# Kernel tuning notes

Hardware: AMD Instinct MI355X
Metric: run time of the kernel (lower is better)

Reference implementation:

```python
import jax, jax.numpy as jnp
import numpy as np

BLOCK = 128


def setup_inputs() -> dict:
    key = jax.random.key(0)
    k_x, k_w, k_s, k_b = jax.random.split(key, 4)
    B, S, IN, OUT = 2, 2048, 4096, 4096
    x = jax.random.normal(k_x, (B, S, IN), dtype=jnp.float32)
    # fp8-quantized weight values (simulate e4m3 rounding, keep fp32 storage)
    w = jax.random.normal(k_w, (OUT, IN), dtype=jnp.float32) * 0.02
    weight = w.astype(jnp.float8_e4m3fn).astype(jnp.float32)
    # per-128x128-block inverse scales
    weight_scale_inv = jax.random.uniform(
        k_s, (OUT // BLOCK, IN // BLOCK), dtype=jnp.float32, minval=0.5, maxval=1.5)
    bias = jax.random.normal(k_b, (OUT,), dtype=jnp.float32) * 0.01
    return {"x": x, "weight": weight, "weight_scale_inv": weight_scale_inv, "bias": bias}


def _dequant(weight, scale_inv):
    # weight: [O, I], scale_inv: [O/128, I/128] -> broadcast each scale over a 128x128 block
    O, I = weight.shape
    w = weight.reshape(O // BLOCK, BLOCK, I // BLOCK, BLOCK)
    w = w * scale_inv[:, None, :, None]
    return w.reshape(O, I)


def reference(x, weight, weight_scale_inv, bias):
    w_deq = _dequant(weight, weight_scale_inv)          # [O, I]
    out = jnp.einsum('bsi,oi->bso', x, w_deq)           # [B, S, O]
    return out + bias
```

## Files before the change

kernel.cpp:

```cpp
#include <hip/hip_runtime.h>
#include <hip/hip_bf16.h>
#include <stdint.h>

typedef __attribute__((ext_vector_type(4))) float f32x4;
typedef __attribute__((ext_vector_type(8))) short short8;

__device__ __forceinline__ ushort f2b(float f) {
    union { __hip_bfloat16 h; ushort u; } c;
    c.h = __float2bfloat16(f);
    return c.u;
}

__device__ __forceinline__ void gload_lds16(const void* g, void* lds) {
    __builtin_amdgcn_global_load_lds((const __attribute__((address_space(1))) void*)g,
                                     (__attribute__((address_space(3))) void*)lds,
                                     16, 0, 0);
}

#define BARRIER()  asm volatile("s_barrier" ::: "memory")
#define LGKM0()    asm volatile("s_waitcnt lgkmcnt(0)" ::: "memory")
#define VMCNT2()   asm volatile("s_waitcnt vmcnt(2)" ::: "memory")

__global__ void conv_x_kernel(const float* __restrict__ x, ushort* __restrict__ xb, long n8) {
    long i = (long)blockIdx.x * blockDim.x + threadIdx.x;
    if (i >= n8) return;
    const float4* xv = (const float4*)x;
    float4 v0 = xv[i * 2], v1 = xv[i * 2 + 1];
    short8 r;
    r[0] = (short)f2b(v0.x); r[1] = (short)f2b(v0.y); r[2] = (short)f2b(v0.z); r[3] = (short)f2b(v0.w);
    r[4] = (short)f2b(v1.x); r[5] = (short)f2b(v1.y); r[6] = (short)f2b(v1.z); r[7] = (short)f2b(v1.w);
    *(short8*)&xb[i * 8] = r;
}

__global__ void conv_w_kernel(const float* __restrict__ w, const float* __restrict__ sinv,
                              ushort* __restrict__ wb, int K, int nbk) {
    const int o = blockIdx.y;
    const int c = (blockIdx.x * blockDim.x + threadIdx.x) * 8;
    if (c >= K) return;
    const float s = sinv[(o >> 7) * nbk + (c >> 7)];
    const float4* wv = (const float4*)(w + (size_t)o * K + c);
    float4 v0 = wv[0], v1 = wv[1];
    short8 r;
    r[0] = (short)f2b(v0.x * s); r[1] = (short)f2b(v0.y * s); r[2] = (short)f2b(v0.z * s); r[3] = (short)f2b(v0.w * s);
    r[4] = (short)f2b(v1.x * s); r[5] = (short)f2b(v1.y * s); r[6] = (short)f2b(v1.z * s); r[7] = (short)f2b(v1.w * s);
    *(short8*)&wb[(size_t)o * K + c] = r;
}

__global__ __launch_bounds__(512, 2)
void gemm256_kernel(const ushort* __restrict__ A, const ushort* __restrict__ Bm,
                    const float* __restrict__ bias, float* __restrict__ C,
                    int M, int N, int K) {
    __shared__ alignas(16) short sm[2][32768];

    const int tid  = threadIdx.x;
    const int lane = tid & 63;
    const int wid  = tid >> 6;
    const int wr   = wid >> 2;
    const int wc   = wid & 3;
    const int nbn  = N >> 8;

    const int nwg = gridDim.x;
    const int swz = (blockIdx.x & 7) * (nwg >> 3) + (blockIdx.x >> 3);
    const int bm  = swz / nbn;
    const int bn  = swz % nbn;

    const short* gA = (const short*)A + (size_t)bm * 256 * K;
    const short* gB = (const short*)Bm + (size_t)bn * 256 * K;

    const int srow = wid * 8 + (lane >> 3);
    const int scol = ((lane & 7) ^ (lane >> 3)) << 3;

    auto STAGE_A = [&](int U, int kt, int buf) {
        const short* src = gA + (size_t)(U * 64 + srow) * K + kt * 64 + scol;
        gload_lds16(src, &sm[buf][U * 4096 + wid * 512]);
    };
    auto STAGE_B = [&](int U, int kt, int buf) {
        const short* src = gB + (size_t)(U * 64 + srow) * K + kt * 64 + scol;
        gload_lds16(src, &sm[buf][16384 + U * 4096 + wid * 512]);
    };

    auto LD_A = [&](const short* Ab, int mh, int kk, short8 (&a)[4]) {
#pragma unroll
        for (int m = 0; m < 4; ++m) {
            int row = wr * 128 + mh * 64 + m * 16 + (lane & 15);
            a[m] = *(const short8*)&Ab[row * 64 + ((kk * 32 + (lane >> 4) * 8) ^ ((lane & 7) << 3))];
        }
    };
    auto LD_B = [&](const short* Bb, int kk, short8 (&b)[4]) {
#pragma unroll
        for (int n = 0; n < 4; ++n) {
            int row = wc * 64 + n * 16 + (lane & 15);
            b[n] = *(const short8*)&Bb[row * 64 + ((kk * 32 + (lane >> 4) * 8) ^ ((lane & 7) << 3))];
        }
    };

    f32x4 acc[8][4] = {};
    const int nkt = K >> 6;

    auto KSTEP = [&](int t) {
        const int b  = t & 1;
        const int tb = b ^ 1;
        const short* Ab = &sm[b][0];
        const short* Bb = &sm[b][16384];
        const int tn  = (t + 1 < nkt) ? t + 1 : nkt - 1;
        const int tnn = (t + 2 < nkt) ? t + 2 : nkt - 1;

        short8 a0[4], a1[4], bf0[4], bf1[4];

        LD_A(Ab, 0, 0, a0);
        LD_B(Bb, 0, bf0);
        STAGE_B(0, tn, tb); STAGE_B(1, tn, tb);
        BARRIER();
        LGKM0();
        __builtin_amdgcn_s_setprio(1);
#pragma unroll
        for (int m = 0; m < 4; ++m)
#pragma unroll
            for (int n = 0; n < 4; ++n)
                acc[m][n] = __builtin_amdgcn_mfma_f32_16x16x32_bf16(a0[m], bf0[n], acc[m][n], 0, 0, 0);
        __builtin_amdgcn_s_setprio(0);
        BARRIER();

        LD_A(Ab, 1, 0, a1);
        STAGE_A(2, tn, tb); STAGE_A(3, tn, tb);
        BARRIER();
        LGKM0();
        __builtin_amdgcn_s_setprio(1);
#pragma unroll
        for (int m = 0; m < 4; ++m)
#pragma unroll
            for (int n = 0; n < 4; ++n)
                acc[4 + m][n] = __builtin_amdgcn_mfma_f32_16x16x32_bf16(a1[m], bf0[n], acc[4 + m][n], 0, 0, 0);
        __builtin_amdgcn_s_setprio(0);
        BARRIER();

        LD_A(Ab, 0, 1, a0);
        LD_B(Bb, 1, bf1);
        STAGE_B(2, tn, tb); STAGE_B(3, tn, tb);
        BARRIER();
        LGKM0();
        __builtin_amdgcn_s_setprio(1);
#pragma unroll
        for (int m = 0; m < 4; ++m)
#pragma unroll
            for (int n = 0; n < 4; ++n)
                acc[m][n] = __builtin_amdgcn_mfma_f32_16x16x32_bf16(a0[m], bf1[n], acc[m][n], 0, 0, 0);
        __builtin_amdgcn_s_setprio(0);
        BARRIER();

        LD_A(Ab, 1, 1, a1);
        STAGE_A(0, tnn, b); STAGE_A(1, tnn, b);
        BARRIER();
        LGKM0();
        __builtin_amdgcn_s_setprio(1);
#pragma unroll
        for (int m = 0; m < 4; ++m)
#pragma unroll
            for (int n = 0; n < 4; ++n)
                acc[4 + m][n] = __builtin_amdgcn_mfma_f32_16x16x32_bf16(a1[m], bf1[n], acc[4 + m][n], 0, 0, 0);
        __builtin_amdgcn_s_setprio(0);
        VMCNT2();
        BARRIER();
    };

    {
        STAGE_B(0, 0, 0); STAGE_B(1, 0, 0);
        STAGE_A(2, 0, 0); STAGE_A(3, 0, 0);
        STAGE_B(2, 0, 0); STAGE_B(3, 0, 0);
        STAGE_A(0, 0, 0); STAGE_A(1, 0, 0);
        const int t1 = (nkt > 1) ? 1 : 0;
        STAGE_A(0, t1, 1); STAGE_A(1, t1, 1);
        VMCNT2();
        BARRIER();
    }

    for (int t = 0; t < nkt; t += 2) {
        KSTEP(t);
        KSTEP(t + 1);
    }

    const int r0 = bm * 256 + wr * 128 + (lane >> 4) * 4;
    const int c0 = bn * 256 + wc * 64 + (lane & 15);
#pragma unroll
    for (int n = 0; n < 4; ++n) {
        float bv = bias[c0 + n * 16];
#pragma unroll
        for (int m = 0; m < 8; ++m) {
#pragma unroll
            for (int r = 0; r < 4; ++r) {
                C[(size_t)(r0 + m * 16 + r) * N + (c0 + n * 16)] = acc[m][n][r] + bv;
            }
        }
    }
}

__global__ void fallback_gemm(const float* __restrict__ x, const float* __restrict__ w,
                              const float* __restrict__ sinv, const float* __restrict__ bias,
                              float* __restrict__ out, int M, int N, int K) {
    int n = blockIdx.x * 64 + (threadIdx.x & 63);
    int m = blockIdx.y * 4 + (threadIdx.x >> 6);
    if (m >= M || n >= N) return;
    const int nbk = K >> 7;
    float acc = 0.f;
    for (int k = 0; k < K; ++k)
        acc += x[(size_t)m * K + k] * w[(size_t)n * K + k] * sinv[(n >> 7) * nbk + (k >> 7)];
    out[(size_t)m * N + n] = acc + bias[n];
}

extern "C" void kernel_launch(void* const* d_in, const int* in_sizes, int n_in,
                              void* d_out, int out_size, void* d_ws, size_t ws_size,
                              hipStream_t stream) {
    const float* x    = (const float*)d_in[0];
    const float* w    = (const float*)d_in[1];
    const float* sinv = (const float*)d_in[2];
    const float* bias = (const float*)d_in[3];
    float* out        = (float*)d_out;

    const int O = in_sizes[3];
    const int K = in_sizes[1] / O;
    const int M = (int)((long)in_sizes[0] / K);
    const int N = O;

    const size_t need = ((size_t)M * K + (size_t)N * K) * sizeof(ushort);
    const int nwg = (M / 256) * (N / 256);
    const bool ok = ws_size >= need && (M % 256 == 0) && (N % 256 == 0) &&
                    (K % 128 == 0) && (nwg % 8 == 0) && ((long)M * K % 2048 == 0) &&
                    (K % 2048 == 0);
    if (ok) {
        ushort* xb = (ushort*)d_ws;
        ushort* wb = xb + (size_t)M * K;
        long n8 = (long)M * K / 8;
        conv_x_kernel<<<dim3((unsigned)(n8 / 256)), 256, 0, stream>>>(x, xb, n8);
        conv_w_kernel<<<dim3(K / 2048, N), 256, 0, stream>>>(w, sinv, wb, K, K >> 7);
        gemm256_kernel<<<dim3(nwg), 512, 0, stream>>>(xb, wb, bias, out, M, N, K);
    } else {
        dim3 g(N / 64, (M + 3) / 4);
        fallback_gemm<<<g, 256, 0, stream>>>(x, w, sinv, bias, out, M, N, K);
    }
}
```

Baseline: 281.4 us.

## Interleave LDS fragment loads with MFMAs and halve barriers per k-step

Rebuilds the GEMM main-loop schedule. Each k-step now uses four barriers instead of eight, and the explicit lgkmcnt(0) waits are gone. LDS fragment reads for the next sub-tile are issued between halves of the current MFMA block, so LDS latency hides behind matrix math. A-tile staging is regrouped so units 0/2 and 1/3 are refilled at the points where they are no longer read. This cuts sync stalls but depends on the compiler's waitcnt insertion and on subtle buffer-reuse ordering staying correct.

```diff
diff --git a/kernel.cpp b/kernel.cpp
--- a/kernel.cpp
+++ b/kernel.cpp
@@ -18,7 +18,6 @@
 }
 
 #define BARRIER()  asm volatile("s_barrier" ::: "memory")
-#define LGKM0()    asm volatile("s_waitcnt lgkmcnt(0)" ::: "memory")
 #define VMCNT2()   asm volatile("s_waitcnt vmcnt(2)" ::: "memory")
 
 __global__ void conv_x_kernel(const float* __restrict__ x, ushort* __restrict__ xb, long n8) {
@@ -95,6 +94,15 @@
     };
 
     f32x4 acc[8][4] = {};
+
+    auto MFMA_H = [&](int off, short8 (&af)[4], short8 (&bf)[4], int m0, int m1) {
+#pragma unroll
+        for (int m = m0; m < m1; ++m)
+#pragma unroll
+            for (int n = 0; n < 4; ++n)
+                acc[off + m][n] = __builtin_amdgcn_mfma_f32_16x16x32_bf16(af[m], bf[n], acc[off + m][n], 0, 0, 0);
+    };
+
     const int nkt = K >> 6;
 
     auto KSTEP = [&](int t) {
@@ -105,73 +113,51 @@
         const int tn  = (t + 1 < nkt) ? t + 1 : nkt - 1;
         const int tnn = (t + 2 < nkt) ? t + 2 : nkt - 1;
 
-        short8 a0[4], a1[4], bf0[4], bf1[4];
-
-        LD_A(Ab, 0, 0, a0);
-        LD_B(Bb, 0, bf0);
+        short8 aA[4], aB[4], aC[4], aD[4], bA[4], bB[4];
+
+        BARRIER();
+        LD_A(Ab, 0, 0, aA);
+        LD_B(Bb, 0, bA);
+        __builtin_amdgcn_s_setprio(1);
+        MFMA_H(0, aA, bA, 0, 2);
+        LD_A(Ab, 1, 0, aB);
+        MFMA_H(0, aA, bA, 2, 4);
+        __builtin_amdgcn_s_setprio(0);
         STAGE_B(0, tn, tb); STAGE_B(1, tn, tb);
-        BARRIER();
-        LGKM0();
-        __builtin_amdgcn_s_setprio(1);
-#pragma unroll
-        for (int m = 0; m < 4; ++m)
-#pragma unroll
-            for (int n = 0; n < 4; ++n)
-                acc[m][n] = __builtin_amdgcn_mfma_f32_16x16x32_bf16(a0[m], bf0[n], acc[m][n], 0, 0, 0);
-        __builtin_amdgcn_s_setprio(0);
-        BARRIER();
-
-        LD_A(Ab, 1, 0, a1);
-        STAGE_A(2, tn, tb); STAGE_A(3, tn, tb);
-        BARRIER();
-        LGKM0();
-        __builtin_amdgcn_s_setprio(1);
-#pragma unroll
-        for (int m = 0; m < 4; ++m)
-#pragma unroll
-            for (int n = 0; n < 4; ++n)
-                acc[4 + m][n] = __builtin_amdgcn_mfma_f32_16x16x32_bf16(a1[m], bf0[n], acc[4 + m][n], 0, 0, 0);
-        __builtin_amdgcn_s_setprio(0);
-        BARRIER();
-
-        LD_A(Ab, 0, 1, a0);
-        LD_B(Bb, 1, bf1);
+
+        BARRIER();
+        __builtin_amdgcn_s_setprio(1);
+        MFMA_H(4, aB, bA, 0, 2);
+        LD_A(Ab, 0, 1, aC);
+        LD_B(Bb, 1, bB);
+        MFMA_H(4, aB, bA, 2, 4);
+        __builtin_amdgcn_s_setprio(0);
+        STAGE_A(1, tn, tb); STAGE_A(3, tn, tb);
+
+        BARRIER();
+        __builtin_amdgcn_s_setprio(1);
+        MFMA_H(0, aC, bB, 0, 2);
+        LD_A(Ab, 1, 1, aD);
+        MFMA_H(0, aC, bB, 2, 4);
+        __builtin_amdgcn_s_setprio(0);
         STAGE_B(2, tn, tb); STAGE_B(3, tn, tb);
-        BARRIER();
-        LGKM0();
-        __builtin_amdgcn_s_setprio(1);
-#pragma unroll
-        for (int m = 0; m < 4; ++m)
-#pragma unroll
-            for (int n = 0; n < 4; ++n)
-                acc[m][n] = __builtin_amdgcn_mfma_f32_16x16x32_bf16(a0[m], bf1[n], acc[m][n], 0, 0, 0);
-        __builtin_amdgcn_s_setprio(0);
-        BARRIER();
-
-        LD_A(Ab, 1, 1, a1);
-        STAGE_A(0, tnn, b); STAGE_A(1, tnn, b);
-        BARRIER();
-        LGKM0();
-        __builtin_amdgcn_s_setprio(1);
-#pragma unroll
-        for (int m = 0; m < 4; ++m)
-#pragma unroll
-            for (int n = 0; n < 4; ++n)
-                acc[4 + m][n] = __builtin_amdgcn_mfma_f32_16x16x32_bf16(a1[m], bf1[n], acc[4 + m][n], 0, 0, 0);
-        __builtin_amdgcn_s_setprio(0);
+
+        BARRIER();
+        __builtin_amdgcn_s_setprio(1);
+        MFMA_H(4, aD, bB, 0, 4);
+        __builtin_amdgcn_s_setprio(0);
+        STAGE_A(0, tnn, b); STAGE_A(2, tnn, b);
         VMCNT2();
-        BARRIER();
     };
 
     {
         STAGE_B(0, 0, 0); STAGE_B(1, 0, 0);
-        STAGE_A(2, 0, 0); STAGE_A(3, 0, 0);
+        STAGE_A(1, 0, 0); STAGE_A(3, 0, 0);
         STAGE_B(2, 0, 0); STAGE_B(3, 0, 0);
-        STAGE_A(0, 0, 0); STAGE_A(1, 0, 0);
+        STAGE_A(0, 0, 0); STAGE_A(2, 0, 0);
         const int t1 = (nkt > 1) ? 1 : 0;
-        STAGE_A(0, t1, 1); STAGE_A(1, t1, 1);
+        STAGE_A(0, t1, 1); STAGE_A(2, t1, 1);
         VMCNT2();
-        BARRIER();
     }
 
     for (int t = 0; t < nkt; t += 2) {
```

New measurement: 279.3 us. Within noise of the previous version (-0.8%).
